# Performance work log

Measured on AMD Instinct MI355X. Metric: run time of the kernel, lower is better.

Reference implementation:

```python
import jax, jax.numpy as jnp
import numpy as np

N_EMBED = 384
NUM_HEADS = 6
KV_HEADS = 3
HEAD_DIM = 64
N_REP = NUM_HEADS // KV_HEADS  # 2
B, T = 8, 2048


def setup_inputs() -> dict:
    key = jax.random.key(0)
    ks = jax.random.split(key, 6)
    s = 0.02
    return {
        "x": jax.random.normal(ks[0], (B, T, N_EMBED), dtype=jnp.float32),
        "attn_mask": jnp.tril(jnp.ones((T, T), dtype=jnp.int32)),
        "Wq_w": jax.random.normal(ks[1], (N_EMBED, N_EMBED), dtype=jnp.float32) * s,
        "Wq_b": jnp.zeros((N_EMBED,), dtype=jnp.float32),
        "Wk_w": jax.random.normal(ks[2], (KV_HEADS * HEAD_DIM, N_EMBED), dtype=jnp.float32) * s,
        "Wk_b": jnp.zeros((KV_HEADS * HEAD_DIM,), dtype=jnp.float32),
        "Wv_w": jax.random.normal(ks[3], (KV_HEADS * HEAD_DIM, N_EMBED), dtype=jnp.float32) * s,
        "Wv_b": jnp.zeros((KV_HEADS * HEAD_DIM,), dtype=jnp.float32),
        "Wo_w": jax.random.normal(ks[4], (N_EMBED, N_EMBED), dtype=jnp.float32) * s,
        "Wo_b": jnp.zeros((N_EMBED,), dtype=jnp.float32),
    }


def reference(x, attn_mask, Wq_w, Wq_b, Wk_w, Wk_b, Wv_w, Wv_b, Wo_w, Wo_b):
    bsz, qlen, _ = x.shape
    # projections (torch Linear: y = x @ W.T + b)
    q = x @ Wq_w.T + Wq_b                              # [B,T,H*D]
    k = x @ Wk_w.T + Wk_b                              # [B,T,KV*D]
    v = x @ Wv_w.T + Wv_b
    q = q.reshape(bsz, qlen, NUM_HEADS, HEAD_DIM).transpose(0, 2, 1, 3)  # [B,H,T,D]
    k = k.reshape(bsz, qlen, KV_HEADS, HEAD_DIM).transpose(0, 2, 1, 3)   # [B,KV,T,D]
    v = v.reshape(bsz, qlen, KV_HEADS, HEAD_DIM).transpose(0, 2, 1, 3)
    # repeat_kv: interleave-expand KV heads to match attention heads
    k = jnp.repeat(k, N_REP, axis=1)                   # [B,H,T,D]
    v = jnp.repeat(v, N_REP, axis=1)
    # NOTE: source scales by 1/sqrt(n_embed), not 1/sqrt(head_dim)
    scale = 1.0 / jnp.sqrt(jnp.float32(N_EMBED))
    scores = jnp.einsum("bhqd,bhkd->bhqk", q, k) * scale
    scores = jnp.where(attn_mask[None, None, :qlen, :qlen] == 0,
                       jnp.float32(-jnp.inf), scores)
    probs = jax.nn.softmax(scores, axis=-1)
    # dropout omitted (deterministic / eval-mode baseline)
    out = jnp.einsum("bhqk,bhkd->bhqd", probs, v)      # [B,H,T,D]
    out = out.transpose(0, 2, 1, 3).reshape(bsz, qlen, N_EMBED)
    return out @ Wo_w.T + Wo_b
```

## Files before the change

### kernel.cpp

```cpp
#include <hip/hip_runtime.h>
#include <cstdint>
#include <cstddef>

#define NE   384
#define NH   6
#define NKV  3
#define HD   64
#define BSZ  8
#define SEQ  2048
#define MROWS (BSZ*SEQ)
#define NT_Q (SEQ/64)

typedef __bf16 bf16x8 __attribute__((ext_vector_type(8)));
typedef __bf16 bf16x4 __attribute__((ext_vector_type(4)));
typedef float  f32x4  __attribute__((ext_vector_type(4)));
typedef unsigned short u16;
typedef u16 u16x8 __attribute__((ext_vector_type(8)));
typedef u16 u16x4 __attribute__((ext_vector_type(4)));

#define MFMA(a,b,c) __builtin_amdgcn_mfma_f32_16x16x32_bf16((a),(b),(c),0,0,0)
#define QSCALE (1.4426950408889634f * 0.05103103630798288f)

__device__ __forceinline__ bf16x8 ld_frag(const u16* lds, int row, int kk) {
    unsigned off = (unsigned)(row*128 + ((kk*2) ^ ((row&7)<<4)));
    return *reinterpret_cast<const bf16x8*>(reinterpret_cast<const char*>(lds) + off);
}
__device__ __forceinline__ void st_frag(u16* lds, int row, int kk, u16x8 v) {
    unsigned off = (unsigned)(row*128 + ((kk*2) ^ ((row&7)<<4)));
    *reinterpret_cast<u16x8*>(reinterpret_cast<char*>(lds) + off) = v;
}
__device__ __forceinline__ bf16x8 ld_fragV(const u16* lds, int row, int kk) {
    unsigned off = (unsigned)(row*128 + ((kk*2) ^ (((row>>1)&7)<<4)));
    return *reinterpret_cast<const bf16x8*>(reinterpret_cast<const char*>(lds) + off);
}
__device__ __forceinline__ void st_fragV(u16* lds, int row, int kk, u16x8 v) {
    unsigned off = (unsigned)(row*128 + ((kk*2) ^ (((row>>1)&7)<<4)));
    *reinterpret_cast<u16x8*>(reinterpret_cast<char*>(lds) + off) = v;
}
__device__ __forceinline__ void st_b64(u16* lds, int row, int col, u16x4 v) {
    unsigned off = (unsigned)(row*128 + ((col*2) ^ ((row&7)<<4)));
    *reinterpret_cast<u16x4*>(reinterpret_cast<char*>(lds) + off) = v;
}
__device__ __forceinline__ u16x4 pack4(f32x4 v) {
    bf16x4 h;
    h[0] = (__bf16)v[0]; h[1] = (__bf16)v[1]; h[2] = (__bf16)v[2]; h[3] = (__bf16)v[3];
    return *reinterpret_cast<u16x4*>(&h);
}

__global__ __launch_bounds__(256) void prep_kernel(
    const float* __restrict__ x,  const float* __restrict__ Wq,
    const float* __restrict__ Wk, const float* __restrict__ Wv,
    const float* __restrict__ Wo,
    __bf16* xb, __bf16* wqb, __bf16* wkb, __bf16* wvb, __bf16* wob)
{
    const float* src; __bf16* dst; int n4;
    switch (blockIdx.y) {
        case 0:  src = x;  dst = xb;  n4 = MROWS*NE/4; break;
        case 1:  src = Wq; dst = wqb; n4 = 384*NE/4;   break;
        case 2:  src = Wk; dst = wkb; n4 = 192*NE/4;   break;
        case 3:  src = Wv; dst = wvb; n4 = 192*NE/4;   break;
        default: src = Wo; dst = wob; n4 = 384*NE/4;   break;
    }
    for (int i = blockIdx.x*256 + threadIdx.x; i < n4; i += gridDim.x*256) {
        float4 v = reinterpret_cast<const float4*>(src)[i];
        bf16x4 h;
        h[0] = (__bf16)v.x; h[1] = (__bf16)v.y; h[2] = (__bf16)v.z; h[3] = (__bf16)v.w;
        reinterpret_cast<bf16x4*>(dst)[i] = h;
    }
}

__global__ __launch_bounds__(256) void qkv_proj_kernel(
    const __bf16* __restrict__ xb,
    const __bf16* __restrict__ wqb, const __bf16* __restrict__ wkb,
    const __bf16* __restrict__ wvb,
    const float* __restrict__ bq, const float* __restrict__ bk,
    const float* __restrict__ bv,
    __bf16* __restrict__ Qb, __bf16* __restrict__ Kb, __bf16* __restrict__ Vb)
{
    __shared__ __align__(16) u16 A_s[64*64], W_s[192*64];

    const int tid = threadIdx.x;
    const int m0 = blockIdx.x * 64;
    const int w  = tid >> 6, l = tid & 63;
    const int lr = l & 15, lg = l >> 4;

    const __bf16* W; const float* bias; int outsel, colbase;
    if (blockIdx.y == 0)      { W = wqb;          bias = bq; outsel = 0; colbase = 0;   }
    else if (blockIdx.y == 1) { W = wqb + 192*NE; bias = bq; outsel = 0; colbase = 192; }
    else if (blockIdx.y == 2) { W = wkb;          bias = bk; outsel = 1; colbase = 0;   }
    else                      { W = wvb;          bias = bv; outsel = 2; colbase = 0;   }

    f32x4 acc[4][3];
    #pragma unroll
    for (int mt = 0; mt < 4; ++mt)
        #pragma unroll
        for (int nt = 0; nt < 3; ++nt) acc[mt][nt] = (f32x4)(0.0f);

    for (int k0 = 0; k0 < NE; k0 += 64) {
        __syncthreads();
        #pragma unroll
        for (int i = 0; i < 2; ++i) {
            int c = tid + i*256, row = c >> 3, c8 = c & 7;
            st_frag(A_s, row, c8*8, *reinterpret_cast<const u16x8*>(&xb[(size_t)(m0+row)*NE + k0 + c8*8]));
        }
        #pragma unroll
        for (int i = 0; i < 6; ++i) {
            int c = tid + i*256, row = c >> 3, c8 = c & 7;
            st_frag(W_s, row, c8*8, *reinterpret_cast<const u16x8*>(&W[(size_t)row*NE + k0 + c8*8]));
        }
        __syncthreads();
        #pragma unroll
        for (int ks = 0; ks < 2; ++ks) {
            bf16x8 ah[4];
            #pragma unroll
            for (int mt = 0; mt < 4; ++mt)
                ah[mt] = ld_frag(A_s, mt*16 + lr, ks*32 + lg*8);
            #pragma unroll
            for (int nt = 0; nt < 3; ++nt) {
                bf16x8 wf = ld_frag(W_s, w*48 + nt*16 + lr, ks*32 + lg*8);
                #pragma unroll
                for (int mt = 0; mt < 4; ++mt)
                    acc[mt][nt] = MFMA(ah[mt], wf, acc[mt][nt]);
            }
        }
    }

    #pragma unroll
    for (int nt = 0; nt < 3; ++nt) {
        int colt = colbase + w*48 + nt*16 + lr;
        float bb = bias[colt];
        int hh = colt >> 6, dd = colt & 63;
        #pragma unroll
        for (int mt = 0; mt < 4; ++mt) {
            #pragma unroll
            for (int r = 0; r < 4; ++r) {
                int m = m0 + mt*16 + lg*4 + r;
                int b8 = m >> 11, t = m & 2047;
                float val = acc[mt][nt][r] + bb;
                if (outsel == 0)
                    Qb[(((size_t)b8*NH + hh)*SEQ + t)*HD + dd] = (__bf16)(val * QSCALE);
                else if (outsel == 1)
                    Kb[(((size_t)b8*NKV + hh)*SEQ + t)*HD + dd] = (__bf16)val;
                else
                    Vb[(((size_t)b8*NKV + hh)*SEQ + t)*HD + dd] = (__bf16)val;
            }
        }
    }
}

__global__ __launch_bounds__(256) void attn_kernel(
    const __bf16* __restrict__ Qb, const __bf16* __restrict__ Kb,
    const __bf16* __restrict__ Vb, __bf16* __restrict__ Ab)
{
    __shared__ __align__(16) u16 Qs[64*64];
    __shared__ __align__(16) u16 Kbuf[2][64*64];
    __shared__ __align__(16) u16 Vbuf[2][64*64];
    __shared__ __align__(16) u16 Ps[4][16*64];

    const int tid = threadIdx.x;
    const int w  = tid >> 6, l = tid & 63;
    const int lr = l & 15, lg = l >> 4;
    const int p = blockIdx.x, h = blockIdx.y, b = blockIdx.z;
    const int kvh = h >> 1;

    const __bf16* Kbase = Kb + ((size_t)b*NKV + kvh)*SEQ*HD;
    const __bf16* Vbase = Vb + ((size_t)b*NKV + kvh)*SEQ*HD;

    const int vd0 = 2*(tid & 31), vkb = (tid >> 5)*8;

    for (int pass = 0; pass < 2; ++pass) {
        const int qtile = pass ? (NT_Q-1-p) : p;
        const int qt0 = qtile * 64;
        const __bf16* Qbase = Qb + (((size_t)b*NH + h)*SEQ + qt0)*HD;

        #pragma unroll
        for (int i = 0; i < 2; ++i) {
            int c = tid + i*256, row = c >> 3, c8 = c & 7;
            st_frag(Qs, row, c8*8, *reinterpret_cast<const u16x8*>(&Qbase[(size_t)row*HD + c8*8]));
        }
        #pragma unroll
        for (int i = 0; i < 2; ++i) {
            int c = tid + i*256, row = c >> 3, c8 = c & 7;
            st_frag(Kbuf[0], row, c8*8, *reinterpret_cast<const u16x8*>(&Kbase[(size_t)row*HD + c8*8]));
        }
        {
            unsigned vp[8];
            #pragma unroll
            for (int j = 0; j < 8; ++j)
                vp[j] = *reinterpret_cast<const unsigned*>(&Vbase[(size_t)(vkb+j)*HD + vd0]);
            u16x8 r0, r1;
            #pragma unroll
            for (int j = 0; j < 8; ++j) { r0[j] = (u16)(vp[j] & 0xffffu); r1[j] = (u16)(vp[j] >> 16); }
            st_fragV(Vbuf[0], vd0,   vkb, r0);
            st_fragV(Vbuf[0], vd0+1, vkb, r1);
        }
        __syncthreads();

        f32x4 oT[4];
        #pragma unroll
        for (int nt = 0; nt < 4; ++nt) oT[nt] = (f32x4)(0.0f);
        float mrun = -1e30f, lrun = 0.0f;
        const int q_abs = qt0 + w*16 + lr;

        int cur = 0;
        for (int jt = 0; jt <= qtile; ++jt) {
            const bool pre = (jt < qtile);
            u16x8 kpre0, kpre1; unsigned vp[8];
            if (pre) {
                const int jn = (jt+1)*64;
                { int c = tid,     row = c >> 3, c8 = c & 7;
                  kpre0 = *reinterpret_cast<const u16x8*>(&Kbase[(size_t)(jn+row)*HD + c8*8]); }
                { int c = tid+256, row = c >> 3, c8 = c & 7;
                  kpre1 = *reinterpret_cast<const u16x8*>(&Kbase[(size_t)(jn+row)*HD + c8*8]); }
                #pragma unroll
                for (int j = 0; j < 8; ++j)
                    vp[j] = *reinterpret_cast<const unsigned*>(&Vbase[(size_t)(jn+vkb+j)*HD + vd0]);
            }

            const u16* Kc = Kbuf[cur];
            const u16* Vc = Vbuf[cur];

            f32x4 sT[4];
            #pragma unroll
            for (int nt = 0; nt < 4; ++nt) sT[nt] = (f32x4)(0.0f);
            #pragma unroll
            for (int ks = 0; ks < 2; ++ks) {
                bf16x8 qf = ld_frag(Qs, w*16 + lr, ks*32 + lg*8);
                #pragma unroll
                for (int nt = 0; nt < 4; ++nt)
                    sT[nt] = MFMA(ld_frag(Kc, nt*16 + lr, ks*32 + lg*8), qf, sT[nt]);
            }
            if (jt == qtile) {
                const int j0 = jt*64;
                #pragma unroll
                for (int nt = 0; nt < 4; ++nt)
                    #pragma unroll
                    for (int r = 0; r < 4; ++r)
                        if (j0 + nt*16 + lg*4 + r > q_abs) sT[nt][r] = -1e30f;
            }

            float mx = -1e30f;
            #pragma unroll
            for (int nt = 0; nt < 4; ++nt)
                #pragma unroll
                for (int r = 0; r < 4; ++r) mx = fmaxf(mx, sT[nt][r]);
            mx = fmaxf(mx, __shfl_xor(mx, 16));
            mx = fmaxf(mx, __shfl_xor(mx, 32));
            float mnew = fmaxf(mrun, mx);
            float corr = exp2f(mrun - mnew);
            mrun = mnew;
            float rs = 0.0f;
            #pragma unroll
            for (int nt = 0; nt < 4; ++nt)
                #pragma unroll
                for (int r = 0; r < 4; ++r) {
                    float pv = exp2f(sT[nt][r] - mnew);
                    sT[nt][r] = pv;
                    rs += pv;
                }
            rs += __shfl_xor(rs, 16);
            rs += __shfl_xor(rs, 32);
            lrun = lrun*corr + rs;

            u16* P = Ps[w];
            #pragma unroll
            for (int nt = 0; nt < 4; ++nt)
                st_b64(P, lr, nt*16 + lg*4, pack4(sT[nt]));

            #pragma unroll
            for (int nt = 0; nt < 4; ++nt)
                #pragma unroll
                for (int r = 0; r < 4; ++r) oT[nt][r] *= corr;

            #pragma unroll
            for (int ks = 0; ks < 2; ++ks) {
                bf16x8 pf = ld_frag(P, lr, ks*32 + lg*8);
                #pragma unroll
                for (int nt = 0; nt < 4; ++nt)
                    oT[nt] = MFMA(ld_fragV(Vc, nt*16 + lr, ks*32 + lg*8), pf, oT[nt]);
            }

            if (pre) {
                u16* Kd = Kbuf[cur ^ 1];
                u16* Vd = Vbuf[cur ^ 1];
                { int c = tid,     row = c >> 3, c8 = c & 7; st_frag(Kd, row, c8*8, kpre0); }
                { int c = tid+256, row = c >> 3, c8 = c & 7; st_frag(Kd, row, c8*8, kpre1); }
                u16x8 r0, r1;
                #pragma unroll
                for (int j = 0; j < 8; ++j) { r0[j] = (u16)(vp[j] & 0xffffu); r1[j] = (u16)(vp[j] >> 16); }
                st_fragV(Vd, vd0,   vkb, r0);
                st_fragV(Vd, vd0+1, vkb, r1);
            }
            __syncthreads();
            cur ^= 1;
        }

        float inv = 1.0f / lrun;
        int t = qt0 + w*16 + lr;
        size_t base = ((size_t)b*SEQ + t)*NE + h*HD;
        #pragma unroll
        for (int nt = 0; nt < 4; ++nt) {
            f32x4 v;
            #pragma unroll
            for (int r = 0; r < 4; ++r) v[r] = oT[nt][r] * inv;
            *reinterpret_cast<u16x4*>(&Ab[base + nt*16 + lg*4]) = pack4(v);
        }
    }
}

__global__ __launch_bounds__(256) void out_proj_kernel(
    const __bf16* __restrict__ Ab, const __bf16* __restrict__ wob,
    const float* __restrict__ bo, float* __restrict__ out)
{
    __shared__ __align__(16) u16 A_s[64*64], W_s[192*64];

    const int tid = threadIdx.x;
    const int m0 = blockIdx.x * 64;
    const int n0 = blockIdx.y * 192;
    const int w  = tid >> 6, l = tid & 63;
    const int lr = l & 15, lg = l >> 4;
    const __bf16* W = wob + (size_t)n0*NE;

    f32x4 acc[4][3];
    #pragma unroll
    for (int mt = 0; mt < 4; ++mt)
        #pragma unroll
        for (int nt = 0; nt < 3; ++nt) acc[mt][nt] = (f32x4)(0.0f);

    for (int k0 = 0; k0 < NE; k0 += 64) {
        __syncthreads();
        #pragma unroll
        for (int i = 0; i < 2; ++i) {
            int c = tid + i*256, row = c >> 3, c8 = c & 7;
            st_frag(A_s, row, c8*8, *reinterpret_cast<const u16x8*>(&Ab[(size_t)(m0+row)*NE + k0 + c8*8]));
        }
        #pragma unroll
        for (int i = 0; i < 6; ++i) {
            int c = tid + i*256, row = c >> 3, c8 = c & 7;
            st_frag(W_s, row, c8*8, *reinterpret_cast<const u16x8*>(&W[(size_t)row*NE + k0 + c8*8]));
        }
        __syncthreads();
        #pragma unroll
        for (int ks = 0; ks < 2; ++ks) {
            bf16x8 ah[4];
            #pragma unroll
            for (int mt = 0; mt < 4; ++mt)
                ah[mt] = ld_frag(A_s, mt*16 + lr, ks*32 + lg*8);
            #pragma unroll
            for (int nt = 0; nt < 3; ++nt) {
                bf16x8 wf = ld_frag(W_s, w*48 + nt*16 + lr, ks*32 + lg*8);
                #pragma unroll
                for (int mt = 0; mt < 4; ++mt)
                    acc[mt][nt] = MFMA(ah[mt], wf, acc[mt][nt]);
            }
        }
    }

    #pragma unroll
    for (int nt = 0; nt < 3; ++nt) {
        int col = n0 + w*48 + nt*16 + lr;
        float bb = bo[col];
        #pragma unroll
        for (int mt = 0; mt < 4; ++mt)
            #pragma unroll
            for (int r = 0; r < 4; ++r) {
                int m = m0 + mt*16 + lg*4 + r;
                out[(size_t)m*NE + col] = acc[mt][nt][r] + bb;
            }
    }
}

extern "C" void kernel_launch(void* const* d_in, const int* in_sizes, int n_in,
                              void* d_out, int out_size, void* d_ws, size_t ws_size,
                              hipStream_t stream)
{
    const float* x  = (const float*)d_in[0];
    const float* Wq = (const float*)d_in[2];
    const float* bq = (const float*)d_in[3];
    const float* Wk = (const float*)d_in[4];
    const float* bk = (const float*)d_in[5];
    const float* Wv = (const float*)d_in[6];
    const float* bv = (const float*)d_in[7];
    const float* Wo = (const float*)d_in[8];
    const float* bo = (const float*)d_in[9];
    float* out = (float*)d_out;

    __bf16* xb  = (__bf16*)d_ws;
    __bf16* wqb = xb  + (size_t)MROWS*NE;
    __bf16* wkb = wqb + 384*NE;
    __bf16* wvb = wkb + 192*NE;
    __bf16* wob = wvb + 192*NE;
    __bf16* Qb  = wob + 384*NE;
    __bf16* Kb  = Qb + (size_t)BSZ*NH*SEQ*HD;
    __bf16* Vb  = Kb + (size_t)BSZ*NKV*SEQ*HD;
    __bf16* Ab  = xb;

    prep_kernel<<<dim3(256, 5), 256, 0, stream>>>(x, Wq, Wk, Wv, Wo,
                                                  xb, wqb, wkb, wvb, wob);
    qkv_proj_kernel<<<dim3(MROWS/64, 4), 256, 0, stream>>>(
        xb, wqb, wkb, wvb, bq, bk, bv, Qb, Kb, Vb);
    attn_kernel<<<dim3(NT_Q/2, NH, BSZ), 256, 0, stream>>>(Qb, Kb, Vb, Ab);
    out_proj_kernel<<<dim3(MROWS/64, 2), 256, 0, stream>>>(Ab, wob, bo, out);
}
```

Before: 210.1 us.

## Store V transposed, keep Q in registers, lazy softmax rescale, smaller GEMM tiles

The QKV projection now writes V in a transposed [d, t] layout, so the attention kernel can load V tiles with plain 16-byte loads instead of gathering 32-bit words and repacking them. Q fragments are held in registers rather than staged through LDS. The online softmax skips rescaling until the running max rises by more than 8, and the row sum is computed with an MFMA against a ones vector. The projection GEMMs use 32-row tiles to launch more blocks, at the cost of reloading the weight tile more often.

```diff
diff --git a/kernel.cpp b/kernel.cpp
--- a/kernel.cpp
+++ b/kernel.cpp
@@ -29,14 +29,6 @@
     unsigned off = (unsigned)(row*128 + ((kk*2) ^ ((row&7)<<4)));
     *reinterpret_cast<u16x8*>(reinterpret_cast<char*>(lds) + off) = v;
 }
-__device__ __forceinline__ bf16x8 ld_fragV(const u16* lds, int row, int kk) {
-    unsigned off = (unsigned)(row*128 + ((kk*2) ^ (((row>>1)&7)<<4)));
-    return *reinterpret_cast<const bf16x8*>(reinterpret_cast<const char*>(lds) + off);
-}
-__device__ __forceinline__ void st_fragV(u16* lds, int row, int kk, u16x8 v) {
-    unsigned off = (unsigned)(row*128 + ((kk*2) ^ (((row>>1)&7)<<4)));
-    *reinterpret_cast<u16x8*>(reinterpret_cast<char*>(lds) + off) = v;
-}
 __device__ __forceinline__ void st_b64(u16* lds, int row, int col, u16x4 v) {
     unsigned off = (unsigned)(row*128 + ((col*2) ^ ((row&7)<<4)));
     *reinterpret_cast<u16x4*>(reinterpret_cast<char*>(lds) + off) = v;
@@ -75,12 +67,12 @@
     const __bf16* __restrict__ wvb,
     const float* __restrict__ bq, const float* __restrict__ bk,
     const float* __restrict__ bv,
-    __bf16* __restrict__ Qb, __bf16* __restrict__ Kb, __bf16* __restrict__ Vb)
-{
-    __shared__ __align__(16) u16 A_s[64*64], W_s[192*64];
+    __bf16* __restrict__ Qb, __bf16* __restrict__ Kb, __bf16* __restrict__ Vt)
+{
+    __shared__ __align__(16) u16 A_s[32*64], W_s[192*64];
 
     const int tid = threadIdx.x;
-    const int m0 = blockIdx.x * 64;
+    const int m0 = blockIdx.x * 32;
     const int w  = tid >> 6, l = tid & 63;
     const int lr = l & 15, lg = l >> 4;
 
@@ -90,17 +82,16 @@
     else if (blockIdx.y == 2) { W = wkb;          bias = bk; outsel = 1; colbase = 0;   }
     else                      { W = wvb;          bias = bv; outsel = 2; colbase = 0;   }
 
-    f32x4 acc[4][3];
-    #pragma unroll
-    for (int mt = 0; mt < 4; ++mt)
+    f32x4 acc[2][3];
+    #pragma unroll
+    for (int mt = 0; mt < 2; ++mt)
         #pragma unroll
         for (int nt = 0; nt < 3; ++nt) acc[mt][nt] = (f32x4)(0.0f);
 
     for (int k0 = 0; k0 < NE; k0 += 64) {
         __syncthreads();
-        #pragma unroll
-        for (int i = 0; i < 2; ++i) {
-            int c = tid + i*256, row = c >> 3, c8 = c & 7;
+        {
+            int row = tid >> 3, c8 = tid & 7;
             st_frag(A_s, row, c8*8, *reinterpret_cast<const u16x8*>(&xb[(size_t)(m0+row)*NE + k0 + c8*8]));
         }
         #pragma unroll
@@ -111,15 +102,15 @@
         __syncthreads();
         #pragma unroll
         for (int ks = 0; ks < 2; ++ks) {
-            bf16x8 ah[4];
-            #pragma unroll
-            for (int mt = 0; mt < 4; ++mt)
+            bf16x8 ah[2];
+            #pragma unroll
+            for (int mt = 0; mt < 2; ++mt)
                 ah[mt] = ld_frag(A_s, mt*16 + lr, ks*32 + lg*8);
             #pragma unroll
             for (int nt = 0; nt < 3; ++nt) {
                 bf16x8 wf = ld_frag(W_s, w*48 + nt*16 + lr, ks*32 + lg*8);
                 #pragma unroll
-                for (int mt = 0; mt < 4; ++mt)
+                for (int mt = 0; mt < 2; ++mt)
                     acc[mt][nt] = MFMA(ah[mt], wf, acc[mt][nt]);
             }
         }
@@ -131,18 +122,25 @@
         float bb = bias[colt];
         int hh = colt >> 6, dd = colt & 63;
         #pragma unroll
-        for (int mt = 0; mt < 4; ++mt) {
-            #pragma unroll
-            for (int r = 0; r < 4; ++r) {
-                int m = m0 + mt*16 + lg*4 + r;
-                int b8 = m >> 11, t = m & 2047;
-                float val = acc[mt][nt][r] + bb;
-                if (outsel == 0)
-                    Qb[(((size_t)b8*NH + hh)*SEQ + t)*HD + dd] = (__bf16)(val * QSCALE);
-                else if (outsel == 1)
-                    Kb[(((size_t)b8*NKV + hh)*SEQ + t)*HD + dd] = (__bf16)val;
-                else
-                    Vb[(((size_t)b8*NKV + hh)*SEQ + t)*HD + dd] = (__bf16)val;
+        for (int mt = 0; mt < 2; ++mt) {
+            int mbase = m0 + mt*16 + lg*4;
+            int b8 = mbase >> 11, t0 = mbase & 2047;
+            if (outsel == 0) {
+                #pragma unroll
+                for (int r = 0; r < 4; ++r)
+                    Qb[(((size_t)b8*NH + hh)*SEQ + t0 + r)*HD + dd] =
+                        (__bf16)((acc[mt][nt][r] + bb) * QSCALE);
+            } else if (outsel == 1) {
+                #pragma unroll
+                for (int r = 0; r < 4; ++r)
+                    Kb[(((size_t)b8*NKV + hh)*SEQ + t0 + r)*HD + dd] =
+                        (__bf16)(acc[mt][nt][r] + bb);
+            } else {
+                f32x4 v;
+                #pragma unroll
+                for (int r = 0; r < 4; ++r) v[r] = acc[mt][nt][r] + bb;
+                *reinterpret_cast<u16x4*>(
+                    &Vt[(((size_t)b8*NKV + hh)*HD + dd)*SEQ + t0]) = pack4(v);
             }
         }
     }
@@ -150,9 +148,8 @@
 
 __global__ __launch_bounds__(256) void attn_kernel(
     const __bf16* __restrict__ Qb, const __bf16* __restrict__ Kb,
-    const __bf16* __restrict__ Vb, __bf16* __restrict__ Ab)
-{
-    __shared__ __align__(16) u16 Qs[64*64];
+    const __bf16* __restrict__ Vt, __bf16* __restrict__ Ab)
+{
     __shared__ __align__(16) u16 Kbuf[2][64*64];
     __shared__ __align__(16) u16 Vbuf[2][64*64];
     __shared__ __align__(16) u16 Ps[4][16*64];
@@ -164,36 +161,27 @@
     const int kvh = h >> 1;
 
     const __bf16* Kbase = Kb + ((size_t)b*NKV + kvh)*SEQ*HD;
-    const __bf16* Vbase = Vb + ((size_t)b*NKV + kvh)*SEQ*HD;
-
-    const int vd0 = 2*(tid & 31), vkb = (tid >> 5)*8;
+    const __bf16* Vbase = Vt + ((size_t)b*NKV + kvh)*HD*SEQ;
+
+    const int srow = tid >> 3, sc8 = tid & 7;
+
+    bf16x8 ones;
+    #pragma unroll
+    for (int j = 0; j < 8; ++j) ones[j] = (__bf16)1.0f;
 
     for (int pass = 0; pass < 2; ++pass) {
         const int qtile = pass ? (NT_Q-1-p) : p;
         const int qt0 = qtile * 64;
         const __bf16* Qbase = Qb + (((size_t)b*NH + h)*SEQ + qt0)*HD;
 
-        #pragma unroll
-        for (int i = 0; i < 2; ++i) {
-            int c = tid + i*256, row = c >> 3, c8 = c & 7;
-            st_frag(Qs, row, c8*8, *reinterpret_cast<const u16x8*>(&Qbase[(size_t)row*HD + c8*8]));
-        }
-        #pragma unroll
-        for (int i = 0; i < 2; ++i) {
-            int c = tid + i*256, row = c >> 3, c8 = c & 7;
-            st_frag(Kbuf[0], row, c8*8, *reinterpret_cast<const u16x8*>(&Kbase[(size_t)row*HD + c8*8]));
-        }
-        {
-            unsigned vp[8];
-            #pragma unroll
-            for (int j = 0; j < 8; ++j)
-                vp[j] = *reinterpret_cast<const unsigned*>(&Vbase[(size_t)(vkb+j)*HD + vd0]);
-            u16x8 r0, r1;
-            #pragma unroll
-            for (int j = 0; j < 8; ++j) { r0[j] = (u16)(vp[j] & 0xffffu); r1[j] = (u16)(vp[j] >> 16); }
-            st_fragV(Vbuf[0], vd0,   vkb, r0);
-            st_fragV(Vbuf[0], vd0+1, vkb, r1);
-        }
+        const __bf16* qrow = Qbase + (size_t)(w*16 + lr)*HD + lg*8;
+        bf16x8 qf0 = *reinterpret_cast<const bf16x8*>(qrow);
+        bf16x8 qf1 = *reinterpret_cast<const bf16x8*>(qrow + 32);
+
+        st_frag(Kbuf[0], srow, sc8*8, *reinterpret_cast<const u16x8*>(&Kbase[(size_t)srow*HD + sc8*8]));
+        st_frag(Kbuf[0], srow+32, sc8*8, *reinterpret_cast<const u16x8*>(&Kbase[(size_t)(srow+32)*HD + sc8*8]));
+        st_frag(Vbuf[0], srow, sc8*8, *reinterpret_cast<const u16x8*>(&Vbase[(size_t)srow*SEQ + sc8*8]));
+        st_frag(Vbuf[0], srow+32, sc8*8, *reinterpret_cast<const u16x8*>(&Vbase[(size_t)(srow+32)*SEQ + sc8*8]));
         __syncthreads();
 
         f32x4 oT[4];
@@ -205,16 +193,13 @@
         int cur = 0;
         for (int jt = 0; jt <= qtile; ++jt) {
             const bool pre = (jt < qtile);
-            u16x8 kpre0, kpre1; unsigned vp[8];
+            u16x8 kpre0, kpre1, vpre0, vpre1;
             if (pre) {
                 const int jn = (jt+1)*64;
-                { int c = tid,     row = c >> 3, c8 = c & 7;
-                  kpre0 = *reinterpret_cast<const u16x8*>(&Kbase[(size_t)(jn+row)*HD + c8*8]); }
-                { int c = tid+256, row = c >> 3, c8 = c & 7;
-                  kpre1 = *reinterpret_cast<const u16x8*>(&Kbase[(size_t)(jn+row)*HD + c8*8]); }
-                #pragma unroll
-                for (int j = 0; j < 8; ++j)
-                    vp[j] = *reinterpret_cast<const unsigned*>(&Vbase[(size_t)(jn+vkb+j)*HD + vd0]);
+                kpre0 = *reinterpret_cast<const u16x8*>(&Kbase[(size_t)(jn+srow)*HD + sc8*8]);
+                kpre1 = *reinterpret_cast<const u16x8*>(&Kbase[(size_t)(jn+srow+32)*HD + sc8*8]);
+                vpre0 = *reinterpret_cast<const u16x8*>(&Vbase[(size_t)srow*SEQ + jn + sc8*8]);
+                vpre1 = *reinterpret_cast<const u16x8*>(&Vbase[(size_t)(srow+32)*SEQ + jn + sc8*8]);
             }
 
             const u16* Kc = Kbuf[cur];
@@ -224,11 +209,9 @@
             #pragma unroll
             for (int nt = 0; nt < 4; ++nt) sT[nt] = (f32x4)(0.0f);
             #pragma unroll
-            for (int ks = 0; ks < 2; ++ks) {
-                bf16x8 qf = ld_frag(Qs, w*16 + lr, ks*32 + lg*8);
-                #pragma unroll
-                for (int nt = 0; nt < 4; ++nt)
-                    sT[nt] = MFMA(ld_frag(Kc, nt*16 + lr, ks*32 + lg*8), qf, sT[nt]);
+            for (int nt = 0; nt < 4; ++nt) {
+                sT[nt] = MFMA(ld_frag(Kc, nt*16 + lr, lg*8), qf0, sT[nt]);
+                sT[nt] = MFMA(ld_frag(Kc, nt*16 + lr, 32 + lg*8), qf1, sT[nt]);
             }
             if (jt == qtile) {
                 const int j0 = jt*64;
@@ -239,57 +222,52 @@
                         if (j0 + nt*16 + lg*4 + r > q_abs) sT[nt][r] = -1e30f;
             }
 
-            float mx = -1e30f;
-            #pragma unroll
-            for (int nt = 0; nt < 4; ++nt)
-                #pragma unroll
-                for (int r = 0; r < 4; ++r) mx = fmaxf(mx, sT[nt][r]);
+            float mxa = fmaxf(fmaxf(sT[0][0], sT[0][1]), fmaxf(sT[0][2], sT[0][3]));
+            float mxb = fmaxf(fmaxf(sT[1][0], sT[1][1]), fmaxf(sT[1][2], sT[1][3]));
+            float mxc = fmaxf(fmaxf(sT[2][0], sT[2][1]), fmaxf(sT[2][2], sT[2][3]));
+            float mxd = fmaxf(fmaxf(sT[3][0], sT[3][1]), fmaxf(sT[3][2], sT[3][3]));
+            float mx = fmaxf(fmaxf(mxa, mxb), fmaxf(mxc, mxd));
             mx = fmaxf(mx, __shfl_xor(mx, 16));
             mx = fmaxf(mx, __shfl_xor(mx, 32));
-            float mnew = fmaxf(mrun, mx);
-            float corr = exp2f(mrun - mnew);
-            mrun = mnew;
-            float rs = 0.0f;
-            #pragma unroll
-            for (int nt = 0; nt < 4; ++nt)
-                #pragma unroll
-                for (int r = 0; r < 4; ++r) {
-                    float pv = exp2f(sT[nt][r] - mnew);
-                    sT[nt][r] = pv;
-                    rs += pv;
-                }
-            rs += __shfl_xor(rs, 16);
-            rs += __shfl_xor(rs, 32);
-            lrun = lrun*corr + rs;
+
+            if (!__all(mx - mrun <= 8.0f)) {
+                float mnew = fmaxf(mrun, mx);
+                float corr = exp2f(mrun - mnew);
+                mrun = mnew;
+                lrun *= corr;
+                #pragma unroll
+                for (int nt = 0; nt < 4; ++nt)
+                    #pragma unroll
+                    for (int r = 0; r < 4; ++r) oT[nt][r] *= corr;
+            }
 
             u16* P = Ps[w];
             #pragma unroll
-            for (int nt = 0; nt < 4; ++nt)
-                st_b64(P, lr, nt*16 + lg*4, pack4(sT[nt]));
-
-            #pragma unroll
-            for (int nt = 0; nt < 4; ++nt)
-                #pragma unroll
-                for (int r = 0; r < 4; ++r) oT[nt][r] *= corr;
-
+            for (int nt = 0; nt < 4; ++nt) {
+                f32x4 pv;
+                #pragma unroll
+                for (int r = 0; r < 4; ++r) pv[r] = exp2f(sT[nt][r] - mrun);
+                st_b64(P, lr, nt*16 + lg*4, pack4(pv));
+            }
+
+            f32x4 rsacc = (f32x4)(0.0f);
             #pragma unroll
             for (int ks = 0; ks < 2; ++ks) {
                 bf16x8 pf = ld_frag(P, lr, ks*32 + lg*8);
+                rsacc = MFMA(ones, pf, rsacc);
                 #pragma unroll
                 for (int nt = 0; nt < 4; ++nt)
-                    oT[nt] = MFMA(ld_fragV(Vc, nt*16 + lr, ks*32 + lg*8), pf, oT[nt]);
-            }
+                    oT[nt] = MFMA(ld_frag(Vc, nt*16 + lr, ks*32 + lg*8), pf, oT[nt]);
+            }
+            lrun += rsacc[0];
 
             if (pre) {
                 u16* Kd = Kbuf[cur ^ 1];
                 u16* Vd = Vbuf[cur ^ 1];
-                { int c = tid,     row = c >> 3, c8 = c & 7; st_frag(Kd, row, c8*8, kpre0); }
-                { int c = tid+256, row = c >> 3, c8 = c & 7; st_frag(Kd, row, c8*8, kpre1); }
-                u16x8 r0, r1;
-                #pragma unroll
-                for (int j = 0; j < 8; ++j) { r0[j] = (u16)(vp[j] & 0xffffu); r1[j] = (u16)(vp[j] >> 16); }
-                st_fragV(Vd, vd0,   vkb, r0);
-                st_fragV(Vd, vd0+1, vkb, r1);
+                st_frag(Kd, srow,    sc8*8, kpre0);
+                st_frag(Kd, srow+32, sc8*8, kpre1);
+                st_frag(Vd, srow,    sc8*8, vpre0);
+                st_frag(Vd, srow+32, sc8*8, vpre1);
             }
             __syncthreads();
             cur ^= 1;
@@ -312,26 +290,25 @@
     const __bf16* __restrict__ Ab, const __bf16* __restrict__ wob,
     const float* __restrict__ bo, float* __restrict__ out)
 {
-    __shared__ __align__(16) u16 A_s[64*64], W_s[192*64];
+    __shared__ __align__(16) u16 A_s[32*64], W_s[192*64];
 
     const int tid = threadIdx.x;
-    const int m0 = blockIdx.x * 64;
+    const int m0 = blockIdx.x * 32;
     const int n0 = blockIdx.y * 192;
     const int w  = tid >> 6, l = tid & 63;
     const int lr = l & 15, lg = l >> 4;
     const __bf16* W = wob + (size_t)n0*NE;
 
-    f32x4 acc[4][3];
-    #pragma unroll
-    for (int mt = 0; mt < 4; ++mt)
+    f32x4 acc[2][3];
+    #pragma unroll
+    for (int mt = 0; mt < 2; ++mt)
         #pragma unroll
         for (int nt = 0; nt < 3; ++nt) acc[mt][nt] = (f32x4)(0.0f);
 
     for (int k0 = 0; k0 < NE; k0 += 64) {
         __syncthreads();
-        #pragma unroll
-        for (int i = 0; i < 2; ++i) {
-            int c = tid + i*256, row = c >> 3, c8 = c & 7;
+        {
+            int row = tid >> 3, c8 = tid & 7;
             st_frag(A_s, row, c8*8, *reinterpret_cast<const u16x8*>(&Ab[(size_t)(m0+row)*NE + k0 + c8*8]));
         }
         #pragma unroll
@@ -342,15 +319,15 @@
         __syncthreads();
         #pragma unroll
         for (int ks = 0; ks < 2; ++ks) {
-            bf16x8 ah[4];
-            #pragma unroll
-            for (int mt = 0; mt < 4; ++mt)
+            bf16x8 ah[2];
+            #pragma unroll
+            for (int mt = 0; mt < 2; ++mt)
                 ah[mt] = ld_frag(A_s, mt*16 + lr, ks*32 + lg*8);
             #pragma unroll
             for (int nt = 0; nt < 3; ++nt) {
                 bf16x8 wf = ld_frag(W_s, w*48 + nt*16 + lr, ks*32 + lg*8);
                 #pragma unroll
-                for (int mt = 0; mt < 4; ++mt)
+                for (int mt = 0; mt < 2; ++mt)
                     acc[mt][nt] = MFMA(ah[mt], wf, acc[mt][nt]);
             }
         }
@@ -361,7 +338,7 @@
         int col = n0 + w*48 + nt*16 + lr;
         float bb = bo[col];
         #pragma unroll
-        for (int mt = 0; mt < 4; ++mt)
+        for (int mt = 0; mt < 2; ++mt)
             #pragma unroll
             for (int r = 0; r < 4; ++r) {
                 int m = m0 + mt*16 + lg*4 + r;
@@ -392,13 +369,13 @@
     __bf16* wob = wvb + 192*NE;
     __bf16* Qb  = wob + 384*NE;
     __bf16* Kb  = Qb + (size_t)BSZ*NH*SEQ*HD;
-    __bf16* Vb  = Kb + (size_t)BSZ*NKV*SEQ*HD;
+    __bf16* Vt  = Kb + (size_t)BSZ*NKV*SEQ*HD;
     __bf16* Ab  = xb;
 
     prep_kernel<<<dim3(256, 5), 256, 0, stream>>>(x, Wq, Wk, Wv, Wo,
                                                   xb, wqb, wkb, wvb, wob);
-    qkv_proj_kernel<<<dim3(MROWS/64, 4), 256, 0, stream>>>(
-        xb, wqb, wkb, wvb, bq, bk, bv, Qb, Kb, Vb);
-    attn_kernel<<<dim3(NT_Q/2, NH, BSZ), 256, 0, stream>>>(Qb, Kb, Vb, Ab);
-    out_proj_kernel<<<dim3(MROWS/64, 2), 256, 0, stream>>>(Ab, wob, bo, out);
-}
+    qkv_proj_kernel<<<dim3(MROWS/32, 4), 256, 0, stream>>>(
+        xb, wqb, wkb, wvb, bq, bk, bv, Qb, Kb, Vt);
+    attn_kernel<<<dim3(NT_Q/2, NH, BSZ), 256, 0, stream>>>(Qb, Kb, Vt, Ab);
+    out_proj_kernel<<<dim3(MROWS/32, 2), 256, 0, stream>>>(Ab, wob, bo, out);
+}
```

Measured after the change: 202.5 us. -3.6%, faster.
